# Kernel optimization log

Measured on AMD Instinct MI355X. Metric: run time of the kernel, lower is better.

The kernel has to match this reference:

```python
import jax, jax.numpy as jnp
import numpy as np

B, S, H = 4, 1024, 2560          # batch, seq, hidden_size
E, K, F = 32, 6, 1536            # num_experts, top_k, moe_intermediate_size
SHARED_F = 2 * 1536              # moe_num_shared_experts * moe_intermediate_size
NORM_MIN = 1e-12                 # config.moe_norm_min


def setup_inputs() -> dict:
    key = jax.random.key(0)
    ks = jax.random.split(key, 9)
    rnd = lambda k, shape, scale=0.02: jax.random.normal(k, shape, dtype=jnp.float32) * scale
    return {
        "hidden_states": jax.random.normal(ks[0], (B, S, H), dtype=jnp.float32),
        "router_w": rnd(ks[1], (E, H)),              # Ernie4_5_MoeTopKRouter.weight (fp32)
        "router_bias": jnp.zeros((E,), jnp.float32),  # moe_statics.e_score_correction_bias
        "gate_w": rnd(ks[2], (E, H, F)),
        "up_w": rnd(ks[3], (E, H, F)),
        "down_w": rnd(ks[4], (E, F, H)),
        "shared_gate_w": rnd(ks[5], (H, SHARED_F)),
        "shared_up_w": rnd(ks[6], (H, SHARED_F)),
        "shared_down_w": rnd(ks[7], (SHARED_F, H)),
    }


def _mlp(x, gw, uw, dw):
    # Ernie4_5_MoeMLP: down( silu(gate(x)) * up(x) ), no biases
    return (jax.nn.silu(x @ gw) * (x @ uw)) @ dw


def _forward(hidden_states, router_w, router_bias, gate_w, up_w, down_w,
             shared_gate_w, shared_up_w, shared_down_w):
    T = B * S
    xt = hidden_states.reshape(T, H)

    # shared experts path (always-on dense MLP)
    shared_out = _mlp(xt, shared_gate_w, shared_up_w, shared_down_w)

    # router: fp32 linear -> softmax -> (+ correction bias) -> top-k -> renorm
    logits = xt.astype(jnp.float32) @ router_w.T            # [T, E]
    probs = jax.nn.softmax(logits, axis=-1)
    top_w, top_i = jax.lax.top_k(probs + router_bias[None, :], K)  # [T, K]
    top_w = top_w / jnp.clip(jnp.sum(top_w, axis=-1, keepdims=True), NORM_MIN)
    top_w = top_w.astype(hidden_states.dtype)

    # expert combine: loop over the fixed expert set; per-token combine weight
    # cw[t] = sum_k top_w[t,k] * (top_i[t,k] == e)  (matches one-hot dispatch +
    # index_add_ scatter combine of the original)
    out = jnp.zeros_like(xt)
    for e in range(E):
        cw = jnp.sum(jnp.where(top_i == e, top_w, 0.0), axis=-1)  # [T]
        y = _mlp(xt, gate_w[e], up_w[e], down_w[e])               # [T, H]
        out = out + cw[:, None] * y

    out = out + shared_out
    return out.reshape(B, S, H)


def reference(hidden_states, router_w, router_bias, gate_w, up_w, down_w,
              shared_gate_w, shared_up_w, shared_down_w):
    return _forward(hidden_states, router_w, router_bias, gate_w, up_w, down_w,
                    shared_gate_w, shared_up_w, shared_down_w)
```

## Files before the change

kernel.cpp:

```cpp
#include <hip/hip_runtime.h>
#include <hip/hip_bf16.h>
#include <math.h>

#define T_TOK 4096
#define HID   2560
#define NEXP  32
#define KTOP  6
#define FF    1536
#define SFF   3072
#define MAXP  (T_TOK*KTOP)

typedef __attribute__((ext_vector_type(8))) short short8;
typedef __attribute__((ext_vector_type(4))) float f32x4;

static __device__ __forceinline__ unsigned short f2bf(float x){
  return __builtin_bit_cast(unsigned short, (__bf16)x);
}

static __device__ __forceinline__ void gload_lds16(const void* g, void* l){
  __builtin_amdgcn_global_load_lds(
      (const __attribute__((address_space(1))) unsigned int*)g,
      (__attribute__((address_space(3))) unsigned int*)l, 16, 0, 0);
}

__global__ void k_cast_x(const float* __restrict__ x, unsigned short* __restrict__ xb){
  int i = (blockIdx.x * 256 + threadIdx.x) * 4;
  float4 v = *(const float4*)(x + i);
  ushort4 o;
  o.x = f2bf(v.x); o.y = f2bf(v.y); o.z = f2bf(v.z); o.w = f2bf(v.w);
  *(ushort4*)(xb + i) = o;
}

__global__ __launch_bounds__(256)
void k_transpose(const float* __restrict__ in, unsigned short* __restrict__ out,
                 const int R, const int C){
  const size_t bo = (size_t)blockIdx.z * (size_t)R * C;
  __shared__ unsigned short t2[64][68];
  const int r0 = blockIdx.y * 64, c0 = blockIdx.x * 64;
  const int tid = threadIdx.x;
  const int cr = tid & 15;
  const int rr = tid >> 4;
#pragma unroll
  for (int i = 0; i < 4; ++i){
    const int r = rr + 16*i;
    float4 v = *(const float4*)(in + bo + (size_t)(r0 + r)*C + c0 + cr*4);
    ushort4 p;
    p.x = f2bf(v.x); p.y = f2bf(v.y); p.z = f2bf(v.z); p.w = f2bf(v.w);
    *(ushort4*)(&t2[r][cr*4]) = p;
  }
  __syncthreads();
  const int rw = tid & 7;
  const int ro = tid >> 3;
#pragma unroll
  for (int i = 0; i < 2; ++i){
    const int c = ro + 32*i;
    ushort4 a, b;
    a.x = t2[rw*8+0][c]; a.y = t2[rw*8+1][c]; a.z = t2[rw*8+2][c]; a.w = t2[rw*8+3][c];
    b.x = t2[rw*8+4][c]; b.y = t2[rw*8+5][c]; b.z = t2[rw*8+6][c]; b.w = t2[rw*8+7][c];
    unsigned short* op = out + bo + (size_t)(c0 + c)*R + r0 + rw*8;
    *(ushort4*)(op)     = a;
    *(ushort4*)(op + 4) = b;
  }
}

__global__ void k_router(const float* __restrict__ x, const float* __restrict__ rw,
                         const float* __restrict__ rb, float* __restrict__ top_w,
                         int* __restrict__ top_i, int* __restrict__ counts){
  const int lane = threadIdx.x & 63;
  const int wv   = threadIdx.x >> 6;
  const int t    = blockIdx.x * 4 + wv;
  const float* xr = x + (size_t)t * HID;
  float xv[40];
#pragma unroll
  for (int i = 0; i < 40; ++i) xv[i] = xr[lane + 64*i];
  float sc[32];
  for (int e = 0; e < 32; ++e){
    const float* w = rw + (size_t)e * HID;
    float s = 0.f;
#pragma unroll
    for (int i = 0; i < 40; ++i) s = fmaf(xv[i], w[lane + 64*i], s);
#pragma unroll
    for (int o = 32; o; o >>= 1) s += __shfl_xor(s, o);
    sc[e] = s;
  }
  float mx = sc[0];
#pragma unroll
  for (int e = 1; e < 32; ++e) mx = fmaxf(mx, sc[e]);
  float se = 0.f;
#pragma unroll
  for (int e = 0; e < 32; ++e){ sc[e] = expf(sc[e] - mx); se += sc[e]; }
  const float inv = 1.f / se;
#pragma unroll
  for (int e = 0; e < 32; ++e) sc[e] = sc[e] * inv + rb[e];

  unsigned chosen = 0; float swv[KTOP]; int sid[KTOP]; float wsum = 0.f;
#pragma unroll
  for (int k = 0; k < KTOP; ++k){
    float bv = -1e30f; int bi = 0;
#pragma unroll
    for (int e = 0; e < 32; ++e){
      bool ok = !((chosen >> e) & 1u);
      if (ok && sc[e] > bv){ bv = sc[e]; bi = e; }
    }
    chosen |= 1u << bi; swv[k] = bv; sid[k] = bi; wsum += bv;
  }
  const float dn = fmaxf(wsum, 1e-12f);
  if (lane < KTOP){
    top_w[t*KTOP + lane] = swv[lane] / dn;
    top_i[t*KTOP + lane] = sid[lane];
    atomicAdd(counts + sid[lane], 1);
  }
}

__global__ void k_scan(const int* __restrict__ counts, int* __restrict__ offsets){
  if (threadIdx.x == 0){
    int a = 0;
    for (int e = 0; e < NEXP; ++e){ offsets[e] = a; a += counts[e]; }
    offsets[NEXP] = a;
  }
}

__global__ void k_scatter(const int* __restrict__ top_i, const float* __restrict__ top_w,
                          const int* __restrict__ offsets, int* __restrict__ cursor,
                          int* __restrict__ pair_tok, float* __restrict__ pair_w){
  const int t = blockIdx.x * 256 + threadIdx.x;
  if (t >= T_TOK) return;
#pragma unroll
  for (int k = 0; k < KTOP; ++k){
    int e = top_i[t*KTOP + k];
    int pos = offsets[e] + atomicAdd(cursor + e, 1);
    pair_tok[pos] = t;
    pair_w[pos]   = top_w[t*KTOP + k];
  }
}

template<bool EXP>
__global__ __launch_bounds__(256, 3)
void k_gateup2(const unsigned short* __restrict__ A,
               const unsigned short* __restrict__ BgT,
               const unsigned short* __restrict__ BuT,
               unsigned short* __restrict__ outp,
               const int* __restrict__ pair_tok,
               const int* __restrict__ counts, const int* __restrict__ offsets,
               const int N)
{
  constexpr int K = HID;
  constexpr int NT = K / 32;
  int M, base; const unsigned short *Bg, *Bu;
  if (EXP){
    const int e = blockIdx.z;
    M = counts[e]; base = offsets[e];
    const size_t wo = (size_t)e * (size_t)N * K;
    Bg = BgT + wo; Bu = BuT + wo;
  } else { M = T_TOK; base = 0; Bg = BgT; Bu = BuT; }
  const int mt = blockIdx.y;
  if (mt * 128 >= M) return;
  const int n0 = blockIdx.x * 128;

  __shared__ unsigned short As[2][128*32];
  __shared__ unsigned short Bgs[2][128*32];
  __shared__ unsigned short Bus[2][128*32];

  const int tid  = threadIdx.x;
  const int lane = tid & 63;
  const int w    = tid >> 6;
  const int wr = w >> 1, wc = w & 1;

  const int lrow  = lane >> 2;
  const int chunk = lane & 3;
  const unsigned short *aptr[2], *bgptr[2], *buptr[2];
  int sw[2];
#pragma unroll
  for (int i = 0; i < 2; ++i){
    const int r = w*32 + i*16 + lrow;
    sw[i] = (chunk ^ (r & 3)) * 8;
    int ar = min(mt*128 + r, M - 1);
    int arow = EXP ? pair_tok[base + ar] : ar;
    aptr[i]  = A  + (size_t)arow * K;
    bgptr[i] = Bg + (size_t)(n0 + r) * K;
    buptr[i] = Bu + (size_t)(n0 + r) * K;
  }

  const f32x4 zero = {0.f,0.f,0.f,0.f};
  f32x4 accg[4][4], accu[4][4];
#pragma unroll
  for (int m = 0; m < 4; ++m)
#pragma unroll
    for (int n = 0; n < 4; ++n){ accg[m][n] = zero; accu[m][n] = zero; }

  const int am  = wr*64 + (lane & 15);
  const int bn_ = wc*64 + (lane & 15);
  const int fg  = ((lane >> 4) ^ (lane & 3)) * 16;

#define GU_STAGE(cb, k0)                                                   \
  {                                                                        \
    char* asd = (char*)As[cb]  + w*2048;                                   \
    char* bgd = (char*)Bgs[cb] + w*2048;                                   \
    char* bud = (char*)Bus[cb] + w*2048;                                   \
    _Pragma("unroll")                                                      \
    for (int i = 0; i < 2; ++i){                                           \
      gload_lds16(aptr[i]  + (k0) + sw[i], asd + i*1024);                  \
      gload_lds16(bgptr[i] + (k0) + sw[i], bgd + i*1024);                  \
      gload_lds16(buptr[i] + (k0) + sw[i], bud + i*1024);                  \
    }                                                                      \
  }

  GU_STAGE(0, 0)
  __syncthreads();
  int cur = 0;
  for (int t = 0; t < NT; ++t){
    if (t + 1 < NT) GU_STAGE(cur ^ 1, (t + 1) * 32)
    short8 af[4], bgf[4], buf_[4];
#pragma unroll
    for (int m = 0; m < 4; ++m)
      af[m] = *(const short8*)((const char*)As[cur] + (am + m*16)*64 + fg);
#pragma unroll
    for (int n = 0; n < 4; ++n){
      bgf[n]  = *(const short8*)((const char*)Bgs[cur] + (bn_ + n*16)*64 + fg);
      buf_[n] = *(const short8*)((const char*)Bus[cur] + (bn_ + n*16)*64 + fg);
    }
#pragma unroll
    for (int m = 0; m < 4; ++m)
#pragma unroll
      for (int n = 0; n < 4; ++n){
        accg[m][n] = __builtin_amdgcn_mfma_f32_16x16x32_bf16(af[m], bgf[n],  accg[m][n], 0, 0, 0);
        accu[m][n] = __builtin_amdgcn_mfma_f32_16x16x32_bf16(af[m], buf_[n], accu[m][n], 0, 0, 0);
      }
    __syncthreads();
    cur ^= 1;
  }
#undef GU_STAGE

#pragma unroll
  for (int m = 0; m < 4; ++m)
#pragma unroll
    for (int j = 0; j < 4; ++j){
      const int rr = mt*128 + wr*64 + m*16 + (lane >> 4)*4 + j;
      if (rr < M){
        unsigned short* orow = outp + (size_t)(base + rr) * N + n0 + wc*64 + (lane & 15);
#pragma unroll
        for (int n = 0; n < 4; ++n){
          float g = accg[m][n][j], u = accu[m][n][j];
          float s = (g / (1.f + expf(-g))) * u;
          orow[n*16] = f2bf(s);
        }
      }
    }
}

template<bool EXP>
__global__ __launch_bounds__(256, 4)
void k_down2(const unsigned short* __restrict__ Aact, const int K,
             const unsigned short* __restrict__ BT, float* __restrict__ outp,
             const int* __restrict__ pair_tok, const float* __restrict__ pair_w,
             const int* __restrict__ counts, const int* __restrict__ offsets)
{
  constexpr int N = HID;
  int M, base; const unsigned short* Bw;
  if (EXP){
    const int e = blockIdx.z;
    M = counts[e]; base = offsets[e];
    Bw = BT + (size_t)e * (size_t)N * K;
  } else { M = T_TOK; base = 0; Bw = BT; }
  const int mt = blockIdx.y;
  if (mt * 128 >= M) return;
  const int n0 = blockIdx.x * 128;

  __shared__ unsigned short As[2][128*32];
  __shared__ unsigned short Bs[2][128*32];

  const int tid  = threadIdx.x;
  const int lane = tid & 63;
  const int w    = tid >> 6;
  const int wr = w >> 1, wc = w & 1;

  const int lrow  = lane >> 2;
  const int chunk = lane & 3;
  const unsigned short *aptr[2], *bptr[2];
  int sw[2];
#pragma unroll
  for (int i = 0; i < 2; ++i){
    const int r = w*32 + i*16 + lrow;
    sw[i] = (chunk ^ (r & 3)) * 8;
    int ar = min(mt*128 + r, M - 1);
    aptr[i] = Aact + (size_t)(base + ar) * K;
    bptr[i] = Bw + (size_t)(n0 + r) * K;
  }

  const f32x4 zero = {0.f,0.f,0.f,0.f};
  f32x4 acc[4][4];
#pragma unroll
  for (int m = 0; m < 4; ++m)
#pragma unroll
    for (int n = 0; n < 4; ++n) acc[m][n] = zero;

  const int am  = wr*64 + (lane & 15);
  const int bn_ = wc*64 + (lane & 15);
  const int fg  = ((lane >> 4) ^ (lane & 3)) * 16;

#define DN_STAGE(cb, k0)                                                   \
  {                                                                        \
    char* asd = (char*)As[cb] + w*2048;                                    \
    char* bsd = (char*)Bs[cb] + w*2048;                                    \
    _Pragma("unroll")                                                      \
    for (int i = 0; i < 2; ++i){                                           \
      gload_lds16(aptr[i] + (k0) + sw[i], asd + i*1024);                   \
      gload_lds16(bptr[i] + (k0) + sw[i], bsd + i*1024);                   \
    }                                                                      \
  }

  const int NT = K / 32;
  DN_STAGE(0, 0)
  __syncthreads();
  int cur = 0;
  for (int t = 0; t < NT; ++t){
    if (t + 1 < NT) DN_STAGE(cur ^ 1, (t + 1) * 32)
    short8 af[4], bf_[4];
#pragma unroll
    for (int m = 0; m < 4; ++m)
      af[m] = *(const short8*)((const char*)As[cur] + (am + m*16)*64 + fg);
#pragma unroll
    for (int n = 0; n < 4; ++n)
      bf_[n] = *(const short8*)((const char*)Bs[cur] + (bn_ + n*16)*64 + fg);
#pragma unroll
    for (int m = 0; m < 4; ++m)
#pragma unroll
      for (int n = 0; n < 4; ++n)
        acc[m][n] = __builtin_amdgcn_mfma_f32_16x16x32_bf16(af[m], bf_[n], acc[m][n], 0, 0, 0);
    __syncthreads();
    cur ^= 1;
  }
#undef DN_STAGE

#pragma unroll
  for (int m = 0; m < 4; ++m)
#pragma unroll
    for (int j = 0; j < 4; ++j){
      const int rr = mt*128 + wr*64 + m*16 + (lane >> 4)*4 + j;
      if (rr < M){
        if (EXP){
          const int p = base + rr;
          const int tok = pair_tok[p];
          const float pw = pair_w[p];
          float* orow = outp + (size_t)tok * HID + n0 + wc*64 + (lane & 15);
#pragma unroll
          for (int n = 0; n < 4; ++n) atomicAdd(orow + n*16, acc[m][n][j] * pw);
        } else {
          float* orow = outp + (size_t)rr * HID + n0 + wc*64 + (lane & 15);
#pragma unroll
          for (int n = 0; n < 4; ++n) orow[n*16] = acc[m][n][j];
        }
      }
    }
}

extern "C" void kernel_launch(void* const* d_in, const int* in_sizes, int n_in,
                              void* d_out, int out_size, void* d_ws, size_t ws_size,
                              hipStream_t stream)
{
  (void)in_sizes; (void)n_in; (void)out_size; (void)ws_size;
  const float* hid = (const float*)d_in[0];
  const float* rw  = (const float*)d_in[1];
  const float* rb  = (const float*)d_in[2];
  const float* gw  = (const float*)d_in[3];
  const float* uw  = (const float*)d_in[4];
  const float* dw  = (const float*)d_in[5];
  const float* sgw = (const float*)d_in[6];
  const float* suw = (const float*)d_in[7];
  const float* sdw = (const float*)d_in[8];
  float* out = (float*)d_out;

  char* ws = (char*)d_ws;
  size_t o = 0;
  unsigned short* xb   = (unsigned short*)(ws + o); o += (size_t)T_TOK*HID*2;
  unsigned short* act  = (unsigned short*)(ws + o); o += (size_t)MAXP*FF*2;
  unsigned short* sact = (unsigned short*)(ws + o); o += (size_t)T_TOK*SFF*2;
  unsigned short* Wbuf = (unsigned short*)(ws + o);
  unsigned short* gT  = Wbuf;
  unsigned short* uT  = Wbuf + (size_t)NEXP*FF*HID;
  unsigned short* sgT = Wbuf + (size_t)2*NEXP*FF*HID;
  unsigned short* suT = sgT + (size_t)SFF*HID;
  unsigned short* dT  = Wbuf;
  unsigned short* sdT = Wbuf + (size_t)NEXP*FF*HID;
  o += (size_t)2*NEXP*FF*HID*2 + (size_t)2*SFF*HID*2;
  float* top_w    = (float*)(ws + o); o += (size_t)T_TOK*KTOP*4;
  int*   top_i    = (int*)(ws + o);   o += (size_t)T_TOK*KTOP*4;
  float* pair_w   = (float*)(ws + o); o += (size_t)MAXP*4;
  int*   pair_tok = (int*)(ws + o);   o += (size_t)MAXP*4;
  int*   counts   = (int*)(ws + o);   o += NEXP*4;
  int*   offsets  = (int*)(ws + o);   o += (NEXP+1)*4;
  int*   cursor   = (int*)(ws + o);   o += NEXP*4;

  hipMemsetAsync(counts, 0, (NEXP + (NEXP+1) + NEXP) * sizeof(int), stream);

  k_cast_x<<<(T_TOK*HID)/1024, 256, 0, stream>>>(hid, xb);
  k_router<<<T_TOK/4, 256, 0, stream>>>(hid, rw, rb, top_w, top_i, counts);
  k_scan<<<1, 64, 0, stream>>>(counts, offsets);
  k_scatter<<<T_TOK/256, 256, 0, stream>>>(top_i, top_w, offsets, cursor, pair_tok, pair_w);

  k_transpose<<<dim3(FF/64,  HID/64, NEXP), 256, 0, stream>>>(gw,  gT,  HID, FF);
  k_transpose<<<dim3(FF/64,  HID/64, NEXP), 256, 0, stream>>>(uw,  uT,  HID, FF);
  k_transpose<<<dim3(SFF/64, HID/64, 1),    256, 0, stream>>>(sgw, sgT, HID, SFF);
  k_transpose<<<dim3(SFF/64, HID/64, 1),    256, 0, stream>>>(suw, suT, HID, SFF);

  k_gateup2<true><<<dim3(FF/128, T_TOK/128, NEXP), 256, 0, stream>>>(
      xb, gT, uT, act, pair_tok, counts, offsets, FF);
  k_gateup2<false><<<dim3(SFF/128, T_TOK/128, 1), 256, 0, stream>>>(
      xb, sgT, suT, sact, nullptr, nullptr, nullptr, SFF);

  k_transpose<<<dim3(HID/64, FF/64,  NEXP), 256, 0, stream>>>(dw,  dT,  FF,  HID);
  k_transpose<<<dim3(HID/64, SFF/64, 1),    256, 0, stream>>>(sdw, sdT, SFF, HID);

  k_down2<false><<<dim3(HID/128, T_TOK/128, 1), 256, 0, stream>>>(
      sact, SFF, sdT, out, nullptr, nullptr, nullptr, nullptr);
  k_down2<true><<<dim3(HID/128, T_TOK/128, NEXP), 256, 0, stream>>>(
      act, FF, dT, out, pair_tok, pair_w, counts, offsets);
}
```

Measured before the change: 2.225 ms.

## Triple-buffer GEMM LDS pipeline and remap blocks across XCDs

```diff
diff --git a/kernel.cpp b/kernel.cpp
--- a/kernel.cpp
+++ b/kernel.cpp
@@ -35,7 +35,7 @@
 void k_transpose(const float* __restrict__ in, unsigned short* __restrict__ out,
                  const int R, const int C){
   const size_t bo = (size_t)blockIdx.z * (size_t)R * C;
-  __shared__ unsigned short t2[64][68];
+  __shared__ unsigned short t2[64][72];
   const int r0 = blockIdx.y * 64, c0 = blockIdx.x * 64;
   const int tid = threadIdx.x;
   const int cr = tid & 15;
@@ -135,8 +135,8 @@
 }
 
 template<bool EXP>
-__global__ __launch_bounds__(256, 3)
-void k_gateup2(const unsigned short* __restrict__ A,
+__global__ __launch_bounds__(256, 2)
+void k_gateup3(const unsigned short* __restrict__ A,
                const unsigned short* __restrict__ BgT,
                const unsigned short* __restrict__ BuT,
                unsigned short* __restrict__ outp,
@@ -146,20 +146,26 @@
 {
   constexpr int K = HID;
   constexpr int NT = K / 32;
+  const int total = gridDim.x;
+  const int phys  = blockIdx.x;
+  const int logical = (phys & 7) * (total >> 3) + (phys >> 3);
+  const int mt   = logical & 31;
+  const int rest = logical >> 5;
+  const int ntiles = N >> 7;
+  const int n0 = (rest % ntiles) << 7;
+
   int M, base; const unsigned short *Bg, *Bu;
   if (EXP){
-    const int e = blockIdx.z;
+    const int e = rest / ntiles;
     M = counts[e]; base = offsets[e];
     const size_t wo = (size_t)e * (size_t)N * K;
     Bg = BgT + wo; Bu = BuT + wo;
   } else { M = T_TOK; base = 0; Bg = BgT; Bu = BuT; }
-  const int mt = blockIdx.y;
   if (mt * 128 >= M) return;
-  const int n0 = blockIdx.x * 128;
-
-  __shared__ unsigned short As[2][128*32];
-  __shared__ unsigned short Bgs[2][128*32];
-  __shared__ unsigned short Bus[2][128*32];
+
+  __shared__ unsigned short As[3][4096];
+  __shared__ unsigned short Bgs[3][4096];
+  __shared__ unsigned short Bus[3][4096];
 
   const int tid  = threadIdx.x;
   const int lane = tid & 63;
@@ -206,18 +212,21 @@
   }
 
   GU_STAGE(0, 0)
-  __syncthreads();
-  int cur = 0;
+  GU_STAGE(1, 32)
+  asm volatile("s_waitcnt vmcnt(6)" ::: "memory");
+  __builtin_amdgcn_s_barrier();
+
+  int c0 = 0, c1 = 1, c2 = 2;
   for (int t = 0; t < NT; ++t){
-    if (t + 1 < NT) GU_STAGE(cur ^ 1, (t + 1) * 32)
+    if (t + 2 < NT) GU_STAGE(c2, (t + 2) * 32)
     short8 af[4], bgf[4], buf_[4];
 #pragma unroll
     for (int m = 0; m < 4; ++m)
-      af[m] = *(const short8*)((const char*)As[cur] + (am + m*16)*64 + fg);
+      af[m] = *(const short8*)((const char*)As + c0*8192 + (am + m*16)*64 + fg);
 #pragma unroll
     for (int n = 0; n < 4; ++n){
-      bgf[n]  = *(const short8*)((const char*)Bgs[cur] + (bn_ + n*16)*64 + fg);
-      buf_[n] = *(const short8*)((const char*)Bus[cur] + (bn_ + n*16)*64 + fg);
+      bgf[n]  = *(const short8*)((const char*)Bgs + c0*8192 + (bn_ + n*16)*64 + fg);
+      buf_[n] = *(const short8*)((const char*)Bus + c0*8192 + (bn_ + n*16)*64 + fg);
     }
 #pragma unroll
     for (int m = 0; m < 4; ++m)
@@ -226,8 +235,10 @@
         accg[m][n] = __builtin_amdgcn_mfma_f32_16x16x32_bf16(af[m], bgf[n],  accg[m][n], 0, 0, 0);
         accu[m][n] = __builtin_amdgcn_mfma_f32_16x16x32_bf16(af[m], buf_[n], accu[m][n], 0, 0, 0);
       }
-    __syncthreads();
-    cur ^= 1;
+    if (t + 2 < NT) asm volatile("s_waitcnt vmcnt(6)" ::: "memory");
+    else            asm volatile("s_waitcnt vmcnt(0)" ::: "memory");
+    __builtin_amdgcn_s_barrier();
+    int tmp = c0; c0 = c1; c1 = c2; c2 = tmp;
   }
 #undef GU_STAGE
 
@@ -249,25 +260,31 @@
 }
 
 template<bool EXP>
-__global__ __launch_bounds__(256, 4)
-void k_down2(const unsigned short* __restrict__ Aact, const int K,
+__global__ __launch_bounds__(256, 3)
+void k_down3(const unsigned short* __restrict__ Aact, const int K,
              const unsigned short* __restrict__ BT, float* __restrict__ outp,
              const int* __restrict__ pair_tok, const float* __restrict__ pair_w,
              const int* __restrict__ counts, const int* __restrict__ offsets)
 {
   constexpr int N = HID;
+  constexpr int ntiles = N >> 7;
+  const int total = gridDim.x;
+  const int phys  = blockIdx.x;
+  const int logical = (phys & 7) * (total >> 3) + (phys >> 3);
+  const int mt   = logical & 31;
+  const int rest = logical >> 5;
+  const int n0 = (rest % ntiles) << 7;
+
   int M, base; const unsigned short* Bw;
   if (EXP){
-    const int e = blockIdx.z;
+    const int e = rest / ntiles;
     M = counts[e]; base = offsets[e];
     Bw = BT + (size_t)e * (size_t)N * K;
   } else { M = T_TOK; base = 0; Bw = BT; }
-  const int mt = blockIdx.y;
   if (mt * 128 >= M) return;
-  const int n0 = blockIdx.x * 128;
-
-  __shared__ unsigned short As[2][128*32];
-  __shared__ unsigned short Bs[2][128*32];
+
+  __shared__ unsigned short As[3][4096];
+  __shared__ unsigned short Bs[3][4096];
 
   const int tid  = threadIdx.x;
   const int lane = tid & 63;
@@ -311,24 +328,29 @@
 
   const int NT = K / 32;
   DN_STAGE(0, 0)
-  __syncthreads();
-  int cur = 0;
+  DN_STAGE(1, 32)
+  asm volatile("s_waitcnt vmcnt(4)" ::: "memory");
+  __builtin_amdgcn_s_barrier();
+
+  int c0 = 0, c1 = 1, c2 = 2;
   for (int t = 0; t < NT; ++t){
-    if (t + 1 < NT) DN_STAGE(cur ^ 1, (t + 1) * 32)
+    if (t + 2 < NT) DN_STAGE(c2, (t + 2) * 32)
     short8 af[4], bf_[4];
 #pragma unroll
     for (int m = 0; m < 4; ++m)
-      af[m] = *(const short8*)((const char*)As[cur] + (am + m*16)*64 + fg);
+      af[m] = *(const short8*)((const char*)As + c0*8192 + (am + m*16)*64 + fg);
 #pragma unroll
     for (int n = 0; n < 4; ++n)
-      bf_[n] = *(const short8*)((const char*)Bs[cur] + (bn_ + n*16)*64 + fg);
+      bf_[n] = *(const short8*)((const char*)Bs + c0*8192 + (bn_ + n*16)*64 + fg);
 #pragma unroll
     for (int m = 0; m < 4; ++m)
 #pragma unroll
       for (int n = 0; n < 4; ++n)
         acc[m][n] = __builtin_amdgcn_mfma_f32_16x16x32_bf16(af[m], bf_[n], acc[m][n], 0, 0, 0);
-    __syncthreads();
-    cur ^= 1;
+    if (t + 2 < NT) asm volatile("s_waitcnt vmcnt(4)" ::: "memory");
+    else            asm volatile("s_waitcnt vmcnt(0)" ::: "memory");
+    __builtin_amdgcn_s_barrier();
+    int tmp = c0; c0 = c1; c1 = c2; c2 = tmp;
   }
 #undef DN_STAGE
 
@@ -403,16 +425,16 @@
   k_transpose<<<dim3(SFF/64, HID/64, 1),    256, 0, stream>>>(sgw, sgT, HID, SFF);
   k_transpose<<<dim3(SFF/64, HID/64, 1),    256, 0, stream>>>(suw, suT, HID, SFF);
 
-  k_gateup2<true><<<dim3(FF/128, T_TOK/128, NEXP), 256, 0, stream>>>(
+  k_gateup3<true><<<32*(FF/128)*NEXP, 256, 0, stream>>>(
       xb, gT, uT, act, pair_tok, counts, offsets, FF);
-  k_gateup2<false><<<dim3(SFF/128, T_TOK/128, 1), 256, 0, stream>>>(
+  k_gateup3<false><<<32*(SFF/128), 256, 0, stream>>>(
       xb, sgT, suT, sact, nullptr, nullptr, nullptr, SFF);
 
   k_transpose<<<dim3(HID/64, FF/64,  NEXP), 256, 0, stream>>>(dw,  dT,  FF,  HID);
   k_transpose<<<dim3(HID/64, SFF/64, 1),    256, 0, stream>>>(sdw, sdT, SFF, HID);
 
-  k_down2<false><<<dim3(HID/128, T_TOK/128, 1), 256, 0, stream>>>(
+  k_down3<false><<<32*(HID/128), 256, 0, stream>>>(
       sact, SFF, sdT, out, nullptr, nullptr, nullptr, nullptr);
-  k_down2<true><<<dim3(HID/128, T_TOK/128, NEXP), 256, 0, stream>>>(
+  k_down3<true><<<32*(HID/128)*NEXP, 256, 0, stream>>>(
       act, FF, dT, out, pair_tok, pair_w, counts, offsets);
 }
```

Measured after the change: 1.953 ms. -12.2%, faster.
